# Kernel optimization log

Measured on AMD Instinct MI355X. Metric: run time of the kernel, lower is better.

Reference implementation:

```python
import jax, jax.numpy as jnp
import numpy as np

BATCH = 65536
INPUT_DIM = 128
NUM_KNOTS = 10
DEGREE = 3  # n_basis = NUM_KNOTS - DEGREE - 1 = 6


def bspline_basis(x, knots, degree):
    """Cox-de Boor B-spline basis, vectorized over all batch/feature entries.

    x: [B, D] (already clipped into [knots[0], knots[-1]))
    knots: [K] uniform knot vector
    returns: [B, D, K - degree - 1]
    """
    xe = x[..., None]                                            # [B, D, 1]
    # degree-0 indicator basis: [B, D, K-1]
    B = ((xe >= knots[:-1]) & (xe < knots[1:])).astype(x.dtype)
    for d in range(1, degree + 1):
        left_den = knots[d:-1] - knots[:-(d + 1)]                # [K-1-d]
        right_den = knots[d + 1:] - knots[1:-d]                  # [K-1-d]
        safe_l = jnp.where(left_den > 0, left_den, 1.0)
        safe_r = jnp.where(right_den > 0, right_den, 1.0)
        left = jnp.where(left_den > 0, (xe - knots[:-(d + 1)]) / safe_l, 0.0) * B[..., :-1]
        right = jnp.where(right_den > 0, (knots[d + 1:] - xe) / safe_r, 0.0) * B[..., 1:]
        B = left + right                                          # [B, D, K-1-d]
    return B


def setup_inputs() -> dict:
    key = jax.random.key(0)
    k1, k2 = jax.random.split(key)
    x = jax.random.normal(k1, (BATCH, INPUT_DIM), dtype=jnp.float32)
    interaction_weights = jax.random.normal(k2, (INPUT_DIM, INPUT_DIM), dtype=jnp.float32)
    return {"x": x, "interaction_weights": interaction_weights}


def reference(x, interaction_weights):
    # Shared uniform knot vector over [-1, 1], identical across all features
    knots = jnp.linspace(-1.0, 1.0, NUM_KNOTS).astype(x.dtype)
    eps = 1e-6
    xc = jnp.clip(x, knots[0], knots[-1] - eps)
    basis = bspline_basis(xc, knots, DEGREE)                     # [B, D, 6]
    B_sz = x.shape[0]
    basis_flat = basis.reshape(B_sz, -1)                         # [B, D*6]
    # interaction: out[b, j] = sum_i x[b,i]^2 * sigmoid(W[i,j])
    # (equivalent to bmm(x^T, x * sigmoid(W)) in the original, without
    #  materializing the [B, D, D] broadcast intermediate)
    S = jax.nn.sigmoid(interaction_weights)                      # [D, D]
    interaction = (x * x) @ S                                    # [B, D]
    return jnp.concatenate([basis_flat, interaction], axis=1)    # [B, D*6 + D]
```

## Files before the change

kernel.cpp:

```cpp
#include <hip/hip_runtime.h>
#include <math.h>

#define BATCH 65536
#define DIM 128
#define NBAS 6
#define OUTW 896
#define ROWS_PER_TILE 64
#define LDS_STRIDE 68

__global__ __launch_bounds__(256) void sigmoid_k(const float* __restrict__ W,
                                                 float* __restrict__ S) {
    int t = blockIdx.x * 256 + threadIdx.x;
    float w = W[t];
    S[t] = 1.0f / (1.0f + expf(-w));
}

__device__ __forceinline__ void bw(float x, int& s,
                                   float& w0, float& w1, float& w2, float& w3) {
    const float i6 = 0.16666666666666666f;
    float xc = fminf(fmaxf(x, -1.0f), 1.0f - 1e-6f);
    float p  = (xc + 1.0f) * 4.5f;
    float sf = floorf(p);
    float u  = p - sf;
    s = (int)sf;
    float u2 = u * u;
    float v  = 1.0f - u;
    w0 = u * u2 * i6;
    w1 = (((-3.0f * u + 3.0f) * u + 3.0f) * u + 1.0f) * i6;
    w2 = ((3.0f * u - 6.0f) * u2 + 4.0f) * i6;
    w3 = v * v * v * i6;
}

__device__ __forceinline__ float pick4(float w0, float w1, float w2, float w3, int d) {
    float r = 0.0f;
    r = (d == 0) ? w0 : r;
    r = (d == 1) ? w1 : r;
    r = (d == 2) ? w2 : r;
    r = (d == 3) ? w3 : r;
    return r;
}

__global__ __launch_bounds__(256, 4) void kan_main(const float* __restrict__ X,
                                                   const float* __restrict__ S,
                                                   float* __restrict__ out) {
    __shared__ __align__(16) float xsqT[DIM * LDS_STRIDE];

    const int tid = threadIdx.x;
    const int row0 = blockIdx.x * ROWS_PER_TILE;

    const float4* X4 = (const float4*)(X + (size_t)row0 * DIM);
#pragma unroll
    for (int k = 0; k < 8; ++k) {
        int e4 = k * 256 + tid;
        int e = e4 * 4;
        int r = e >> 7;
        int i = e & 127;
        float4 xv = X4[e4];
        xsqT[(i + 0) * LDS_STRIDE + r] = xv.x * xv.x;
        xsqT[(i + 1) * LDS_STRIDE + r] = xv.y * xv.y;
        xsqT[(i + 2) * LDS_STRIDE + r] = xv.z * xv.z;
        xsqT[(i + 3) * LDS_STRIDE + r] = xv.w * xv.w;
    }
    __syncthreads();

    {
        const int c = tid & 31;
        const int rg = tid >> 5;
        const int r0 = rg * 8;

        float acc[8][4];
#pragma unroll
        for (int rr = 0; rr < 8; ++rr)
#pragma unroll
            for (int q = 0; q < 4; ++q) acc[rr][q] = 0.0f;

        const float4* S4 = (const float4*)S;
#pragma unroll 4
        for (int i = 0; i < DIM; ++i) {
            float4 s = S4[i * 32 + c];
            const float4* xr4 = (const float4*)&xsqT[i * LDS_STRIDE + r0];
            float4 xa = xr4[0];
            float4 xb = xr4[1];
            float xr[8] = {xa.x, xa.y, xa.z, xa.w, xb.x, xb.y, xb.z, xb.w};
#pragma unroll
            for (int rr = 0; rr < 8; ++rr) {
#pragma unroll
                for (int q = 0; q < 4; ++q) {
                    float sv = (q == 0) ? s.x : (q == 1) ? s.y : (q == 2) ? s.z : s.w;
                    acc[rr][q] = fmaf(xr[rr], sv, acc[rr][q]);
                }
            }
        }

#pragma unroll
        for (int rr = 0; rr < 8; ++rr) {
            float4* o = (float4*)(out + (size_t)(row0 + r0 + rr) * OUTW + DIM * NBAS + 4 * c);
            *o = make_float4(acc[rr][0], acc[rr][1], acc[rr][2], acc[rr][3]);
        }
    }

    {
        const int wv = tid >> 6;
        const int lane = tid & 63;
#pragma unroll 2
        for (int n = 0; n < 48; ++n) {
            unsigned wt = (unsigned)(n * 4 + wv);
            unsigned r = wt / 3u;
            unsigned third = wt - 3u * r;
            unsigned j = third * 64u + (unsigned)lane;
            unsigned m = j % 3u;
            unsigned o0 = 4u * j;
            unsigned fA = o0 / 6u;
            unsigned fB = (fA < 127u) ? fA + 1u : 127u;

            const float* xrow = X + (size_t)(row0 + r) * DIM;
            float xA = xrow[fA];
            float xB = xrow[fB];

            int sA, sB;
            float a0, a1, a2, a3, b0, b1, b2, b3;
            bw(xA, sA, a0, a1, a2, a3);
            bw(xB, sB, b0, b1, b2, b3);

            int tb = (m == 0u) ? 0 : (m == 2u) ? 2 : 4;
            int dA = sA - tb;

            float r0v = pick4(a0, a1, a2, a3, dA);
            float r1v = pick4(a0, a1, a2, a3, dA - 1);
            float r2v = (m == 1u) ? pick4(b0, b1, b2, b3, sB)
                                  : pick4(a0, a1, a2, a3, dA - 2);
            float r3v = (m == 1u) ? pick4(b0, b1, b2, b3, sB - 1)
                                  : pick4(a0, a1, a2, a3, dA - 3);

            float4* o = (float4*)(out + (size_t)(row0 + r) * OUTW + o0);
            *o = make_float4(r0v, r1v, r2v, r3v);
        }
    }
}

extern "C" void kernel_launch(void* const* d_in, const int* in_sizes, int n_in,
                              void* d_out, int out_size, void* d_ws, size_t ws_size,
                              hipStream_t stream) {
    const float* X = (const float*)d_in[0];
    const float* W = (const float*)d_in[1];
    float* out = (float*)d_out;
    float* S = (float*)d_ws;

    sigmoid_k<<<(DIM * DIM) / 256, 256, 0, stream>>>(W, S);
    kan_main<<<BATCH / ROWS_PER_TILE, 256, 0, stream>>>(X, S, out);
}
```

Baseline: 294.7 us.

## Read basis inputs from LDS tile and alternate gemm/basis phase order across blocks

The LDS tile now stores raw x instead of x squared. The squaring moves into the GEMM inner loop, which adds 8 multiplies per iteration. The basis phase now reads x from LDS instead of re-reading global memory, and it hoists the per-lane index math (divisions and modulo) out of the row loop. Groups of 256 blocks alternate which phase runs first, so compute-heavy and store-heavy phases interleave across concurrent blocks. The risks are the extra multiplies, LDS bank conflicts on the transposed reads in the basis phase, and more register pressure from the hoisted offsets.

Result: no change. 291.8 us (-1.0%).

```diff
diff --git a/kernel.cpp b/kernel.cpp
--- a/kernel.cpp
+++ b/kernel.cpp
@@ -40,10 +40,95 @@
     return r;
 }
 
+__device__ __forceinline__ void do_gemm(const float* __restrict__ xT,
+                                        const float* __restrict__ S,
+                                        float* __restrict__ out,
+                                        int row0, int tid) {
+    const int c = tid & 31;
+    const int rg = tid >> 5;
+    const int r0 = rg * 8;
+
+    float acc[8][4];
+#pragma unroll
+    for (int rr = 0; rr < 8; ++rr)
+#pragma unroll
+        for (int q = 0; q < 4; ++q) acc[rr][q] = 0.0f;
+
+    const float4* S4 = (const float4*)S;
+#pragma unroll 4
+    for (int i = 0; i < DIM; ++i) {
+        float4 s = S4[i * 32 + c];
+        const float4* xr4 = (const float4*)&xT[i * LDS_STRIDE + r0];
+        float4 xa = xr4[0];
+        float4 xb = xr4[1];
+        float xr[8] = {xa.x * xa.x, xa.y * xa.y, xa.z * xa.z, xa.w * xa.w,
+                       xb.x * xb.x, xb.y * xb.y, xb.z * xb.z, xb.w * xb.w};
+#pragma unroll
+        for (int rr = 0; rr < 8; ++rr) {
+#pragma unroll
+            for (int q = 0; q < 4; ++q) {
+                float sv = (q == 0) ? s.x : (q == 1) ? s.y : (q == 2) ? s.z : s.w;
+                acc[rr][q] = fmaf(xr[rr], sv, acc[rr][q]);
+            }
+        }
+    }
+
+#pragma unroll
+    for (int rr = 0; rr < 8; ++rr) {
+        float4* o = (float4*)(out + (size_t)(row0 + r0 + rr) * OUTW + DIM * NBAS + 4 * c);
+        *o = make_float4(acc[rr][0], acc[rr][1], acc[rr][2], acc[rr][3]);
+    }
+}
+
+__device__ __forceinline__ void do_basis(const float* __restrict__ xT,
+                                         float* __restrict__ out,
+                                         int row0, int tid) {
+    const int lane = tid & 63;
+    const int wv = tid >> 6;
+
+    int offA[3], offB[3], tb[3];
+    bool useB[3];
+#pragma unroll
+    for (int t = 0; t < 3; ++t) {
+        int j = t * 64 + lane;
+        int m = j % 3;
+        int o0 = 4 * j;
+        int fA = o0 / 6;
+        int fB = (fA < 127) ? fA + 1 : 127;
+        offA[t] = fA * LDS_STRIDE;
+        offB[t] = fB * LDS_STRIDE;
+        tb[t] = (m == 0) ? 0 : (m == 2) ? 2 : 4;
+        useB[t] = (m == 1);
+    }
+
+#pragma unroll 2
+    for (int rr = 0; rr < 16; ++rr) {
+        int r = rr * 4 + wv;
+        float4* orow4 = (float4*)(out + (size_t)(row0 + r) * OUTW);
+#pragma unroll
+        for (int t = 0; t < 3; ++t) {
+            float xA = xT[offA[t] + r];
+            float xB = xT[offB[t] + r];
+            int sA, sB;
+            float a0, a1, a2, a3, b0, b1, b2, b3;
+            bw(xA, sA, a0, a1, a2, a3);
+            bw(xB, sB, b0, b1, b2, b3);
+            int dA = sA - tb[t];
+            float r0v = pick4(a0, a1, a2, a3, dA);
+            float r1v = pick4(a0, a1, a2, a3, dA - 1);
+            float r2v = useB[t] ? pick4(b0, b1, b2, b3, sB)
+                                : pick4(a0, a1, a2, a3, dA - 2);
+            float r3v = useB[t] ? pick4(b0, b1, b2, b3, sB - 1)
+                                : pick4(a0, a1, a2, a3, dA - 3);
+            orow4[t * 64 + lane] = make_float4(r0v, r1v, r2v, r3v);
+        }
+    }
+}
+
 __global__ __launch_bounds__(256, 4) void kan_main(const float* __restrict__ X,
                                                    const float* __restrict__ S,
                                                    float* __restrict__ out) {
-    __shared__ __align__(16) float xsqT[DIM * LDS_STRIDE];
+    __shared__ __align__(16) float xT[DIM * LDS_STRIDE];
 
     const int tid = threadIdx.x;
     const int row0 = blockIdx.x * ROWS_PER_TILE;
@@ -56,85 +141,19 @@
         int r = e >> 7;
         int i = e & 127;
         float4 xv = X4[e4];
-        xsqT[(i + 0) * LDS_STRIDE + r] = xv.x * xv.x;
-        xsqT[(i + 1) * LDS_STRIDE + r] = xv.y * xv.y;
-        xsqT[(i + 2) * LDS_STRIDE + r] = xv.z * xv.z;
-        xsqT[(i + 3) * LDS_STRIDE + r] = xv.w * xv.w;
+        xT[(i + 0) * LDS_STRIDE + r] = xv.x;
+        xT[(i + 1) * LDS_STRIDE + r] = xv.y;
+        xT[(i + 2) * LDS_STRIDE + r] = xv.z;
+        xT[(i + 3) * LDS_STRIDE + r] = xv.w;
     }
     __syncthreads();
 
-    {
-        const int c = tid & 31;
-        const int rg = tid >> 5;
-        const int r0 = rg * 8;
-
-        float acc[8][4];
-#pragma unroll
-        for (int rr = 0; rr < 8; ++rr)
-#pragma unroll
-            for (int q = 0; q < 4; ++q) acc[rr][q] = 0.0f;
-
-        const float4* S4 = (const float4*)S;
-#pragma unroll 4
-        for (int i = 0; i < DIM; ++i) {
-            float4 s = S4[i * 32 + c];
-            const float4* xr4 = (const float4*)&xsqT[i * LDS_STRIDE + r0];
-            float4 xa = xr4[0];
-            float4 xb = xr4[1];
-            float xr[8] = {xa.x, xa.y, xa.z, xa.w, xb.x, xb.y, xb.z, xb.w};
-#pragma unroll
-            for (int rr = 0; rr < 8; ++rr) {
-#pragma unroll
-                for (int q = 0; q < 4; ++q) {
-                    float sv = (q == 0) ? s.x : (q == 1) ? s.y : (q == 2) ? s.z : s.w;
-                    acc[rr][q] = fmaf(xr[rr], sv, acc[rr][q]);
-                }
-            }
-        }
-
-#pragma unroll
-        for (int rr = 0; rr < 8; ++rr) {
-            float4* o = (float4*)(out + (size_t)(row0 + r0 + rr) * OUTW + DIM * NBAS + 4 * c);
-            *o = make_float4(acc[rr][0], acc[rr][1], acc[rr][2], acc[rr][3]);
-        }
-    }
-
-    {
-        const int wv = tid >> 6;
-        const int lane = tid & 63;
-#pragma unroll 2
-        for (int n = 0; n < 48; ++n) {
-            unsigned wt = (unsigned)(n * 4 + wv);
-            unsigned r = wt / 3u;
-            unsigned third = wt - 3u * r;
-            unsigned j = third * 64u + (unsigned)lane;
-            unsigned m = j % 3u;
-            unsigned o0 = 4u * j;
-            unsigned fA = o0 / 6u;
-            unsigned fB = (fA < 127u) ? fA + 1u : 127u;
-
-            const float* xrow = X + (size_t)(row0 + r) * DIM;
-            float xA = xrow[fA];
-            float xB = xrow[fB];
-
-            int sA, sB;
-            float a0, a1, a2, a3, b0, b1, b2, b3;
-            bw(xA, sA, a0, a1, a2, a3);
-            bw(xB, sB, b0, b1, b2, b3);
-
-            int tb = (m == 0u) ? 0 : (m == 2u) ? 2 : 4;
-            int dA = sA - tb;
-
-            float r0v = pick4(a0, a1, a2, a3, dA);
-            float r1v = pick4(a0, a1, a2, a3, dA - 1);
-            float r2v = (m == 1u) ? pick4(b0, b1, b2, b3, sB)
-                                  : pick4(a0, a1, a2, a3, dA - 2);
-            float r3v = (m == 1u) ? pick4(b0, b1, b2, b3, sB - 1)
-                                  : pick4(a0, a1, a2, a3, dA - 3);
-
-            float4* o = (float4*)(out + (size_t)(row0 + r) * OUTW + o0);
-            *o = make_float4(r0v, r1v, r2v, r3v);
-        }
+    if (((blockIdx.x >> 8) & 1) == 0) {
+        do_gemm(xT, S, out, row0, tid);
+        do_basis(xT, out, row0, tid);
+    } else {
+        do_basis(xT, out, row0, tid);
+        do_gemm(xT, S, out, row0, tid);
     }
 }
 
```

## Halve tile rows, read basis inputs from LDS, use nontemporal stores

Applied to the files above, without the earlier changes.

The row tile shrinks from 64 to 32 rows, and X is staged in LDS row-major (padded stride) instead of as transposed squares. The basis stage now reads x from LDS instead of re-reading global memory, and its per-lane index math is hoisted out of the row loop. Output writes use nontemporal stores to avoid polluting cache. The GEMV part does fewer FMAs per thread and reads four scalar LDS values per iteration, so data reuse drops while occupancy rises through launch bounds of 8.

Result: no change. 290.5 us (-1.4%).

```diff
diff --git a/kernel.cpp b/kernel.cpp
--- a/kernel.cpp
+++ b/kernel.cpp
@@ -5,8 +5,11 @@
 #define DIM 128
 #define NBAS 6
 #define OUTW 896
-#define ROWS_PER_TILE 64
-#define LDS_STRIDE 68
+#define ROWS_PER_TILE 32
+#define LDS_F4 33
+#define LDS_F 132
+
+typedef float f4v __attribute__((ext_vector_type(4)));
 
 __global__ __launch_bounds__(256) void sigmoid_k(const float* __restrict__ W,
                                                  float* __restrict__ S) {
@@ -40,100 +43,104 @@
     return r;
 }
 
-__global__ __launch_bounds__(256, 4) void kan_main(const float* __restrict__ X,
+__global__ __launch_bounds__(256, 8) void kan_main(const float* __restrict__ X,
                                                    const float* __restrict__ S,
                                                    float* __restrict__ out) {
-    __shared__ __align__(16) float xsqT[DIM * LDS_STRIDE];
+    __shared__ __align__(16) float xTf[ROWS_PER_TILE * LDS_F];
 
     const int tid = threadIdx.x;
     const int row0 = blockIdx.x * ROWS_PER_TILE;
 
     const float4* X4 = (const float4*)(X + (size_t)row0 * DIM);
+    float4* xT4 = (float4*)xTf;
 #pragma unroll
-    for (int k = 0; k < 8; ++k) {
+    for (int k = 0; k < 4; ++k) {
         int e4 = k * 256 + tid;
-        int e = e4 * 4;
-        int r = e >> 7;
-        int i = e & 127;
-        float4 xv = X4[e4];
-        xsqT[(i + 0) * LDS_STRIDE + r] = xv.x * xv.x;
-        xsqT[(i + 1) * LDS_STRIDE + r] = xv.y * xv.y;
-        xsqT[(i + 2) * LDS_STRIDE + r] = xv.z * xv.z;
-        xsqT[(i + 3) * LDS_STRIDE + r] = xv.w * xv.w;
+        int r = e4 >> 5;
+        int i4 = e4 & 31;
+        xT4[r * LDS_F4 + i4] = X4[e4];
     }
     __syncthreads();
 
     {
         const int c = tid & 31;
-        const int rg = tid >> 5;
-        const int r0 = rg * 8;
+        const int r0 = (tid >> 5) * 4;
 
-        float acc[8][4];
+        float acc[4][4];
 #pragma unroll
-        for (int rr = 0; rr < 8; ++rr)
+        for (int rr = 0; rr < 4; ++rr)
 #pragma unroll
             for (int q = 0; q < 4; ++q) acc[rr][q] = 0.0f;
 
         const float4* S4 = (const float4*)S;
-#pragma unroll 4
+        const float* xp0 = xTf + (r0 + 0) * LDS_F;
+        const float* xp1 = xTf + (r0 + 1) * LDS_F;
+        const float* xp2 = xTf + (r0 + 2) * LDS_F;
+        const float* xp3 = xTf + (r0 + 3) * LDS_F;
+#pragma unroll 2
         for (int i = 0; i < DIM; ++i) {
             float4 s = S4[i * 32 + c];
-            const float4* xr4 = (const float4*)&xsqT[i * LDS_STRIDE + r0];
-            float4 xa = xr4[0];
-            float4 xb = xr4[1];
-            float xr[8] = {xa.x, xa.y, xa.z, xa.w, xb.x, xb.y, xb.z, xb.w};
+            float x0 = xp0[i], x1 = xp1[i], x2 = xp2[i], x3 = xp3[i];
+            float xq[4] = {x0 * x0, x1 * x1, x2 * x2, x3 * x3};
 #pragma unroll
-            for (int rr = 0; rr < 8; ++rr) {
+            for (int rr = 0; rr < 4; ++rr) {
 #pragma unroll
                 for (int q = 0; q < 4; ++q) {
                     float sv = (q == 0) ? s.x : (q == 1) ? s.y : (q == 2) ? s.z : s.w;
-                    acc[rr][q] = fmaf(xr[rr], sv, acc[rr][q]);
+                    acc[rr][q] = fmaf(xq[rr], sv, acc[rr][q]);
                 }
             }
         }
 
 #pragma unroll
-        for (int rr = 0; rr < 8; ++rr) {
-            float4* o = (float4*)(out + (size_t)(row0 + r0 + rr) * OUTW + DIM * NBAS + 4 * c);
-            *o = make_float4(acc[rr][0], acc[rr][1], acc[rr][2], acc[rr][3]);
+        for (int rr = 0; rr < 4; ++rr) {
+            f4v v = {acc[rr][0], acc[rr][1], acc[rr][2], acc[rr][3]};
+            __builtin_nontemporal_store(
+                v, (f4v*)(out + (size_t)(row0 + r0 + rr) * OUTW + DIM * NBAS + 4 * c));
         }
     }
 
     {
+        const int lane = tid & 63;
         const int wv = tid >> 6;
-        const int lane = tid & 63;
+
+        int fAh[3], fBh[3], tbh[3];
+        bool uBh[3];
+#pragma unroll
+        for (int t = 0; t < 3; ++t) {
+            int j = t * 64 + lane;
+            int m = j % 3;
+            int o0 = 4 * j;
+            int fA = o0 / 6;
+            fAh[t] = fA;
+            fBh[t] = (fA < 127) ? fA + 1 : 127;
+            tbh[t] = (m == 0) ? 0 : (m == 2) ? 2 : 4;
+            uBh[t] = (m == 1);
+        }
+
 #pragma unroll 2
-        for (int n = 0; n < 48; ++n) {
-            unsigned wt = (unsigned)(n * 4 + wv);
-            unsigned r = wt / 3u;
-            unsigned third = wt - 3u * r;
-            unsigned j = third * 64u + (unsigned)lane;
-            unsigned m = j % 3u;
-            unsigned o0 = 4u * j;
-            unsigned fA = o0 / 6u;
-            unsigned fB = (fA < 127u) ? fA + 1u : 127u;
-
-            const float* xrow = X + (size_t)(row0 + r) * DIM;
-            float xA = xrow[fA];
-            float xB = xrow[fB];
-
-            int sA, sB;
-            float a0, a1, a2, a3, b0, b1, b2, b3;
-            bw(xA, sA, a0, a1, a2, a3);
-            bw(xB, sB, b0, b1, b2, b3);
-
-            int tb = (m == 0u) ? 0 : (m == 2u) ? 2 : 4;
-            int dA = sA - tb;
-
-            float r0v = pick4(a0, a1, a2, a3, dA);
-            float r1v = pick4(a0, a1, a2, a3, dA - 1);
-            float r2v = (m == 1u) ? pick4(b0, b1, b2, b3, sB)
-                                  : pick4(a0, a1, a2, a3, dA - 2);
-            float r3v = (m == 1u) ? pick4(b0, b1, b2, b3, sB - 1)
-                                  : pick4(a0, a1, a2, a3, dA - 3);
-
-            float4* o = (float4*)(out + (size_t)(row0 + r) * OUTW + o0);
-            *o = make_float4(r0v, r1v, r2v, r3v);
+        for (int rr = 0; rr < 8; ++rr) {
+            int r = rr * 4 + wv;
+            const float* xrow = xTf + r * LDS_F;
+            float* orow = out + (size_t)(row0 + r) * OUTW;
+#pragma unroll
+            for (int t = 0; t < 3; ++t) {
+                float xA = xrow[fAh[t]];
+                float xB = xrow[fBh[t]];
+                int sA, sB;
+                float a0, a1, a2, a3, b0, b1, b2, b3;
+                bw(xA, sA, a0, a1, a2, a3);
+                bw(xB, sB, b0, b1, b2, b3);
+                int dA = sA - tbh[t];
+                float r0v = pick4(a0, a1, a2, a3, dA);
+                float r1v = pick4(a0, a1, a2, a3, dA - 1);
+                float r2v = uBh[t] ? pick4(b0, b1, b2, b3, sB)
+                                   : pick4(a0, a1, a2, a3, dA - 2);
+                float r3v = uBh[t] ? pick4(b0, b1, b2, b3, sB - 1)
+                                   : pick4(a0, a1, a2, a3, dA - 3);
+                f4v v = {r0v, r1v, r2v, r3v};
+                __builtin_nontemporal_store(v, (f4v*)(orow + 4 * (t * 64 + lane)));
+            }
         }
     }
 }
```
